# Kernel tuning notes

Hardware: AMD Instinct MI355X
Metric: run time of the kernel (lower is better)

The kernel has to match this reference:

```python
import jax, jax.numpy as jnp
import numpy as np

IN_FEATURES = 4096
OUT_FEATURES = 16384
BATCH = 2
SEQ = 2048


def setup_inputs() -> dict:
    key = jax.random.key(0)
    k_x, k_s, k_sgn, k_b = jax.random.split(key, 4)
    x = jax.random.normal(k_x, (BATCH, SEQ, IN_FEATURES), dtype=jnp.float32)
    # stored: uint8-style inverse-log magnitudes in [1, 255]
    stored = jax.random.randint(k_s, (OUT_FEATURES, IN_FEATURES), 1, 256, dtype=jnp.int32)
    # sign in {0,1}; mapped to {-1,+1} inside reference
    sign = jax.random.randint(k_sgn, (OUT_FEATURES, IN_FEATURES), 0, 2, dtype=jnp.int32)
    # log range matching typical weight magnitudes exp(-8)..exp(0)
    log_min = jnp.full((1,), -8.0, dtype=jnp.float32)
    log_max = jnp.full((1,), 0.0, dtype=jnp.float32)
    bias = jax.random.normal(k_b, (OUT_FEATURES,), dtype=jnp.float32) * 0.02
    return {"x": x, "stored": stored, "sign": sign, "log_min": log_min,
            "log_max": log_max, "bias": bias}


def _dequant_qins(stored, sign, log_min, log_max):
    # reverse inverse mapping: stored in [1,255] -> normalized in [0,1]
    normalized = (255.0 - stored.astype(jnp.float32)) / 254.0
    log_weight = log_min + normalized * (log_max - log_min)
    sign_f = (2 * sign - 1).astype(jnp.float32)  # {0,1} -> {-1,+1}
    return sign_f * jnp.exp(log_weight)  # [out, in] fp32


def reference(x, stored, sign, log_min, log_max, bias):
    lmin = log_min[0]
    lmax = log_max[0]
    w = _dequant_qins(stored, sign, lmin, lmax)  # [O, I]
    # F.linear: y = x @ w.T + bias
    out = jnp.einsum('bsi,oi->bso', x, w) + bias
    return out
```

## Files before the change

### kernel.cpp

```cpp
#include <hip/hip_runtime.h>
#include <stdint.h>

#define M_DIM 4096
#define N_DIM 16384
#define K_DIM 4096
#define BM 256
#define BN 256
#define BK 64
#define NT (K_DIM / BK)

typedef __attribute__((ext_vector_type(8))) __bf16 bf16x8;
typedef __attribute__((ext_vector_type(4))) float f32x4;

__device__ __forceinline__ unsigned short f2bf(float f) {
    uint32_t u = __builtin_bit_cast(uint32_t, f);
    uint32_t r = (u + 0x7FFFu + ((u >> 16) & 1u)) >> 16;
    return (unsigned short)r;
}

union Pack8 { unsigned short h[8]; uint4 v; };

__device__ __forceinline__ void async_copy16(const void* g, void* l) {
    __builtin_amdgcn_global_load_lds((__attribute__((address_space(1))) void*)(g),
                                     (__attribute__((address_space(3))) void*)(l),
                                     16, 0, 0);
}

#define BARRIER() do { asm volatile("" ::: "memory"); \
                       __builtin_amdgcn_s_barrier();  \
                       asm volatile("" ::: "memory"); } while (0)

__global__ __launch_bounds__(256) void cast_x_kernel(const float* __restrict__ x,
                                                     unsigned short* __restrict__ xb,
                                                     int n8) {
    for (int i = blockIdx.x * blockDim.x + threadIdx.x; i < n8;
         i += gridDim.x * blockDim.x) {
        const float4* p = (const float4*)(x + (size_t)i * 8);
        float4 v0 = p[0], v1 = p[1];
        Pack8 o;
        o.h[0] = f2bf(v0.x); o.h[1] = f2bf(v0.y);
        o.h[2] = f2bf(v0.z); o.h[3] = f2bf(v0.w);
        o.h[4] = f2bf(v1.x); o.h[5] = f2bf(v1.y);
        o.h[6] = f2bf(v1.z); o.h[7] = f2bf(v1.w);
        *(uint4*)(xb + (size_t)i * 8) = o.v;
    }
}

__global__ __launch_bounds__(256) void dequant_kernel(const int* __restrict__ stored,
                                                      const int* __restrict__ sign,
                                                      const float* __restrict__ log_min,
                                                      const float* __restrict__ log_max,
                                                      unsigned short* __restrict__ wb,
                                                      int n8) {
    const float lmin = log_min[0];
    const float lrange = log_max[0] - lmin;
    for (int i = blockIdx.x * blockDim.x + threadIdx.x; i < n8;
         i += gridDim.x * blockDim.x) {
        const int4* ps = (const int4*)(stored + (size_t)i * 8);
        const int4* pg = (const int4*)(sign + (size_t)i * 8);
        int4 s0 = ps[0], s1 = ps[1];
        int4 g0 = pg[0], g1 = pg[1];
        int sv[8] = {s0.x, s0.y, s0.z, s0.w, s1.x, s1.y, s1.z, s1.w};
        int gv[8] = {g0.x, g0.y, g0.z, g0.w, g1.x, g1.y, g1.z, g1.w};
        Pack8 o;
#pragma unroll
        for (int j = 0; j < 8; ++j) {
            float nrm = (255.0f - (float)sv[j]) * (1.0f / 254.0f);
            float w = __expf(lmin + nrm * lrange);
            o.h[j] = f2bf(gv[j] ? w : -w);
        }
        *(uint4*)(wb + (size_t)i * 8) = o.v;
    }
}

__global__ __launch_bounds__(512, 2) void gemm_kernel(const unsigned short* __restrict__ A,
                                                      const unsigned short* __restrict__ W,
                                                      const float* __restrict__ bias,
                                                      float* __restrict__ C) {
    extern __shared__ char lds[];
    const int tid  = threadIdx.x;
    const int wave = tid >> 6;
    const int lane = tid & 63;
    const int l15  = lane & 15;
    const int l16  = lane >> 4;
    const int wr   = wave >> 2;
    const int wc   = wave & 3;

    const int bid = blockIdx.x;
    const int wg  = ((bid & 7) << 7) | (bid >> 3);
    const int rowBase = (wg >> 6) * BM;
    const int colBase = (wg & 63) * BN;

    f32x4 acc[8][4] = {};

    auto stage_half = [&](int t, int d, int u) {
        const int kb = t * BK;
        const unsigned short* g = (u < 2) ? A : W;
        const int rb = ((u < 2) ? rowBase : colBase) + (u & 1) * 128;
        char* hb = lds + d * 65536 + ((u < 2) ? 0 : 32768) + (u & 1) * 16384;
#pragma unroll
        for (int sub = 0; sub < 2; ++sub) {
            const int Ld   = (sub * 512 + tid) * 16;
            const int r    = Ld >> 7;
            const int colb = (Ld & 127) ^ ((r & 7) << 4);
            async_copy16(g + (size_t)(rb + r) * K_DIM + kb + (colb >> 1),
                         hb + (sub * 512 + wave * 64) * 16);
        }
    };

    stage_half(0, 0, 0); stage_half(0, 0, 1);
    stage_half(0, 0, 2); stage_half(0, 0, 3);
    stage_half(1, 1, 0); stage_half(1, 1, 1);

    for (int t = 0; t < NT; ++t) {
        const int c = t & 1;
        if (t + 1 < NT) asm volatile("s_waitcnt vmcnt(4)" ::: "memory");
        else            asm volatile("s_waitcnt vmcnt(0)" ::: "memory");
        BARRIER();

        const char* bA  = lds + c * 65536 + wr * 16384;
        const char* bB  = lds + c * 65536 + 32768 + (wc >> 1) * 16384;
        const int   brB = (wc & 1) * 64;

        bf16x8 aF0[4][2], aF1[4][2], bF0[2][2], bF1[2][2];

#pragma unroll
        for (int i = 0; i < 4; ++i)
#pragma unroll
            for (int ks = 0; ks < 2; ++ks) {
                const int r    = i * 16 + l15;
                const int colb = (ks * 64 + l16 * 16) ^ ((r & 7) << 4);
                aF0[i][ks] = *(const bf16x8*)(bA + (r << 7) + colb);
            }
#pragma unroll
        for (int j = 0; j < 2; ++j)
#pragma unroll
            for (int ks = 0; ks < 2; ++ks) {
                const int r    = brB + j * 16 + l15;
                const int colb = (ks * 64 + l16 * 16) ^ ((r & 7) << 4);
                bF0[j][ks] = *(const bf16x8*)(bB + (r << 7) + colb);
            }
#pragma unroll
        for (int j = 0; j < 2; ++j)
#pragma unroll
            for (int ks = 0; ks < 2; ++ks) {
                const int r    = brB + 32 + j * 16 + l15;
                const int colb = (ks * 64 + l16 * 16) ^ ((r & 7) << 4);
                bF1[j][ks] = *(const bf16x8*)(bB + (r << 7) + colb);
            }
        if (t + 1 < NT) stage_half(t + 1, c ^ 1, 2);
        __builtin_amdgcn_s_setprio(1);
#pragma unroll
        for (int i = 0; i < 4; ++i)
#pragma unroll
            for (int j = 0; j < 2; ++j)
#pragma unroll
                for (int ks = 0; ks < 2; ++ks)
                    acc[i][j] = __builtin_amdgcn_mfma_f32_16x16x32_bf16(
                        aF0[i][ks], bF0[j][ks], acc[i][j], 0, 0, 0);
        __builtin_amdgcn_s_setprio(0);

#pragma unroll
        for (int i = 0; i < 4; ++i)
#pragma unroll
            for (int ks = 0; ks < 2; ++ks) {
                const int r    = 64 + i * 16 + l15;
                const int colb = (ks * 64 + l16 * 16) ^ ((r & 7) << 4);
                aF1[i][ks] = *(const bf16x8*)(bA + (r << 7) + colb);
            }
        if (t + 1 < NT) stage_half(t + 1, c ^ 1, 3);
        __builtin_amdgcn_s_setprio(1);
#pragma unroll
        for (int i = 0; i < 4; ++i)
#pragma unroll
            for (int j = 0; j < 2; ++j)
#pragma unroll
                for (int ks = 0; ks < 2; ++ks)
                    acc[i][2 + j] = __builtin_amdgcn_mfma_f32_16x16x32_bf16(
                        aF0[i][ks], bF1[j][ks], acc[i][2 + j], 0, 0, 0);
        __builtin_amdgcn_s_setprio(0);

        __builtin_amdgcn_s_setprio(1);
#pragma unroll
        for (int i = 0; i < 4; ++i)
#pragma unroll
            for (int j = 0; j < 2; ++j)
#pragma unroll
                for (int ks = 0; ks < 2; ++ks)
                    acc[4 + i][j] = __builtin_amdgcn_mfma_f32_16x16x32_bf16(
                        aF1[i][ks], bF0[j][ks], acc[4 + i][j], 0, 0, 0);
        __builtin_amdgcn_s_setprio(0);
        BARRIER();

        if (t + 2 < NT) { stage_half(t + 2, c, 0); stage_half(t + 2, c, 1); }
        __builtin_amdgcn_s_setprio(1);
#pragma unroll
        for (int i = 0; i < 4; ++i)
#pragma unroll
            for (int j = 0; j < 2; ++j)
#pragma unroll
                for (int ks = 0; ks < 2; ++ks)
                    acc[4 + i][2 + j] = __builtin_amdgcn_mfma_f32_16x16x32_bf16(
                        aF1[i][ks], bF1[j][ks], acc[4 + i][2 + j], 0, 0, 0);
        __builtin_amdgcn_s_setprio(0);
    }

#pragma unroll
    for (int m = 0; m < 8; ++m) {
        const int grow0 = rowBase + wr * 128 + m * 16 + l16 * 4;
#pragma unroll
        for (int n = 0; n < 4; ++n) {
            const int gcol = colBase + wc * 64 + n * 16 + l15;
            const float bv = bias[gcol];
#pragma unroll
            for (int r4 = 0; r4 < 4; ++r4)
                C[(size_t)(grow0 + r4) * N_DIM + gcol] = acc[m][n][r4] + bv;
        }
    }
}

extern "C" void kernel_launch(void* const* d_in, const int* in_sizes, int n_in,
                              void* d_out, int out_size, void* d_ws, size_t ws_size,
                              hipStream_t stream) {
    const float* x       = (const float*)d_in[0];
    const int*   stored  = (const int*)d_in[1];
    const int*   sign    = (const int*)d_in[2];
    const float* log_min = (const float*)d_in[3];
    const float* log_max = (const float*)d_in[4];
    const float* bias    = (const float*)d_in[5];
    float* out = (float*)d_out;

    unsigned short* Ab = (unsigned short*)d_ws;
    unsigned short* Wb = (unsigned short*)((char*)d_ws +
                          (size_t)M_DIM * K_DIM * sizeof(unsigned short));

    cast_x_kernel<<<2048, 256, 0, stream>>>(x, Ab, (M_DIM * K_DIM) / 8);
    dequant_kernel<<<4096, 256, 0, stream>>>(stored, sign, log_min, log_max, Wb,
                                             (N_DIM * K_DIM) / 8);

    hipFuncSetAttribute((const void*)gemm_kernel,
                        hipFuncAttributeMaxDynamicSharedMemorySize, 131072);
    gemm_kernel<<<dim3((M_DIM / BM) * (N_DIM / BN)), dim3(512), 131072, stream>>>(
        Ab, Wb, bias, out);
}
```

Baseline: 617.9 us.

## Restructure GEMM main loop into barrier-synchronized quadrant phases with shared A fragments

Reworks the K-loop into four phases, each loading one fragment set, issuing one global-to-LDS prefetch half, then synchronizing with explicit lgkmcnt waits, sched_barriers and workgroup barriers before its MFMA block. The A fragments are reused through a single register array instead of two, which lowers register pressure. The prefetch order of the staged halves is changed to match the new phase order. Many more barriers per iteration are added, which can cause stalls, and the staging order has to stay correct for the double-buffer reuse.

```diff
diff --git a/kernel.cpp b/kernel.cpp
--- a/kernel.cpp
+++ b/kernel.cpp
@@ -110,27 +110,25 @@
 
     stage_half(0, 0, 0); stage_half(0, 0, 1);
     stage_half(0, 0, 2); stage_half(0, 0, 3);
-    stage_half(1, 1, 0); stage_half(1, 1, 1);
+    stage_half(1, 1, 2); stage_half(1, 1, 0);
+    asm volatile("s_waitcnt vmcnt(4)" ::: "memory");
+    BARRIER();
+
+    bf16x8 aF[4][2], bF0[2][2], bF1[2][2];
 
     for (int t = 0; t < NT; ++t) {
         const int c = t & 1;
-        if (t + 1 < NT) asm volatile("s_waitcnt vmcnt(4)" ::: "memory");
-        else            asm volatile("s_waitcnt vmcnt(0)" ::: "memory");
-        BARRIER();
-
         const char* bA  = lds + c * 65536 + wr * 16384;
         const char* bB  = lds + c * 65536 + 32768 + (wc >> 1) * 16384;
         const int   brB = (wc & 1) * 64;
 
-        bf16x8 aF0[4][2], aF1[4][2], bF0[2][2], bF1[2][2];
-
 #pragma unroll
         for (int i = 0; i < 4; ++i)
 #pragma unroll
             for (int ks = 0; ks < 2; ++ks) {
                 const int r    = i * 16 + l15;
                 const int colb = (ks * 64 + l16 * 16) ^ ((r & 7) << 4);
-                aF0[i][ks] = *(const bf16x8*)(bA + (r << 7) + colb);
+                aF[i][ks] = *(const bf16x8*)(bA + (r << 7) + colb);
             }
 #pragma unroll
         for (int j = 0; j < 2; ++j)
@@ -140,6 +138,23 @@
                 const int colb = (ks * 64 + l16 * 16) ^ ((r & 7) << 4);
                 bF0[j][ks] = *(const bf16x8*)(bB + (r << 7) + colb);
             }
+        if (t + 1 < NT) stage_half(t + 1, c ^ 1, 1);
+        asm volatile("s_waitcnt lgkmcnt(8)" ::: "memory");
+        BARRIER();
+        asm volatile("s_waitcnt lgkmcnt(0)" ::: "memory");
+        __builtin_amdgcn_sched_barrier(0);
+        __builtin_amdgcn_s_setprio(1);
+#pragma unroll
+        for (int i = 0; i < 4; ++i)
+#pragma unroll
+            for (int j = 0; j < 2; ++j)
+#pragma unroll
+                for (int ks = 0; ks < 2; ++ks)
+                    acc[i][j] = __builtin_amdgcn_mfma_f32_16x16x32_bf16(
+                        aF[i][ks], bF0[j][ks], acc[i][j], 0, 0, 0);
+        __builtin_amdgcn_s_setprio(0);
+        BARRIER();
+
 #pragma unroll
         for (int j = 0; j < 2; ++j)
 #pragma unroll
@@ -148,17 +163,21 @@
                 const int colb = (ks * 64 + l16 * 16) ^ ((r & 7) << 4);
                 bF1[j][ks] = *(const bf16x8*)(bB + (r << 7) + colb);
             }
-        if (t + 1 < NT) stage_half(t + 1, c ^ 1, 2);
-        __builtin_amdgcn_s_setprio(1);
-#pragma unroll
-        for (int i = 0; i < 4; ++i)
-#pragma unroll
-            for (int j = 0; j < 2; ++j)
-#pragma unroll
-                for (int ks = 0; ks < 2; ++ks)
-                    acc[i][j] = __builtin_amdgcn_mfma_f32_16x16x32_bf16(
-                        aF0[i][ks], bF0[j][ks], acc[i][j], 0, 0, 0);
-        __builtin_amdgcn_s_setprio(0);
+        if (t + 1 < NT) stage_half(t + 1, c ^ 1, 3);
+        BARRIER();
+        asm volatile("s_waitcnt lgkmcnt(0)" ::: "memory");
+        __builtin_amdgcn_sched_barrier(0);
+        __builtin_amdgcn_s_setprio(1);
+#pragma unroll
+        for (int i = 0; i < 4; ++i)
+#pragma unroll
+            for (int j = 0; j < 2; ++j)
+#pragma unroll
+                for (int ks = 0; ks < 2; ++ks)
+                    acc[i][2 + j] = __builtin_amdgcn_mfma_f32_16x16x32_bf16(
+                        aF[i][ks], bF1[j][ks], acc[i][2 + j], 0, 0, 0);
+        __builtin_amdgcn_s_setprio(0);
+        BARRIER();
 
 #pragma unroll
         for (int i = 0; i < 4; ++i)
@@ -166,20 +185,12 @@
             for (int ks = 0; ks < 2; ++ks) {
                 const int r    = 64 + i * 16 + l15;
                 const int colb = (ks * 64 + l16 * 16) ^ ((r & 7) << 4);
-                aF1[i][ks] = *(const bf16x8*)(bA + (r << 7) + colb);
-            }
-        if (t + 1 < NT) stage_half(t + 1, c ^ 1, 3);
-        __builtin_amdgcn_s_setprio(1);
-#pragma unroll
-        for (int i = 0; i < 4; ++i)
-#pragma unroll
-            for (int j = 0; j < 2; ++j)
-#pragma unroll
-                for (int ks = 0; ks < 2; ++ks)
-                    acc[i][2 + j] = __builtin_amdgcn_mfma_f32_16x16x32_bf16(
-                        aF0[i][ks], bF1[j][ks], acc[i][2 + j], 0, 0, 0);
-        __builtin_amdgcn_s_setprio(0);
-
+                aF[i][ks] = *(const bf16x8*)(bA + (r << 7) + colb);
+            }
+        if (t + 2 < NT) stage_half(t + 2, c, 2);
+        BARRIER();
+        asm volatile("s_waitcnt lgkmcnt(0)" ::: "memory");
+        __builtin_amdgcn_sched_barrier(0);
         __builtin_amdgcn_s_setprio(1);
 #pragma unroll
         for (int i = 0; i < 4; ++i)
@@ -188,11 +199,18 @@
 #pragma unroll
                 for (int ks = 0; ks < 2; ++ks)
                     acc[4 + i][j] = __builtin_amdgcn_mfma_f32_16x16x32_bf16(
-                        aF1[i][ks], bF0[j][ks], acc[4 + i][j], 0, 0, 0);
-        __builtin_amdgcn_s_setprio(0);
-        BARRIER();
-
-        if (t + 2 < NT) { stage_half(t + 2, c, 0); stage_half(t + 2, c, 1); }
+                        aF[i][ks], bF0[j][ks], acc[4 + i][j], 0, 0, 0);
+        __builtin_amdgcn_s_setprio(0);
+        BARRIER();
+
+        if (t + 2 < NT) {
+            stage_half(t + 2, c, 0);
+            asm volatile("s_waitcnt vmcnt(4)" ::: "memory");
+        } else {
+            asm volatile("s_waitcnt vmcnt(0)" ::: "memory");
+        }
+        BARRIER();
+        __builtin_amdgcn_sched_barrier(0);
         __builtin_amdgcn_s_setprio(1);
 #pragma unroll
         for (int i = 0; i < 4; ++i)
@@ -201,8 +219,9 @@
 #pragma unroll
                 for (int ks = 0; ks < 2; ++ks)
                     acc[4 + i][2 + j] = __builtin_amdgcn_mfma_f32_16x16x32_bf16(
-                        aF1[i][ks], bF1[j][ks], acc[4 + i][2 + j], 0, 0, 0);
-        __builtin_amdgcn_s_setprio(0);
+                        aF[i][ks], bF1[j][ks], acc[4 + i][2 + j], 0, 0, 0);
+        __builtin_amdgcn_s_setprio(0);
+        BARRIER();
     }
 
 #pragma unroll
```

Measured after the change: 623.8 us. About the same (+1.0%).
